# Kernel tuning notes

Measured on AMD Instinct MI355X. Metric: run time of the kernel, lower is better.

The kernel has to match this reference:

```python
import jax, jax.numpy as jnp
import numpy as np

NHEAD = 4
DIM = 256

def rotate_half(x):
    # interleaved: out[..., ::2] = -x[..., 1::2]; out[..., 1::2] = x[..., ::2]
    xe = x[..., ::2]
    xo = x[..., 1::2]
    return jnp.stack([-xo, xe], axis=-1).reshape(x.shape)

def rope_2d(q, k, H, W):
    Dh = q.shape[-1]
    half = Dh // 2
    inv_freq = 1.0 / (10000.0 ** (jnp.arange(half, dtype=jnp.float32) / half))  # [half]
    yy, xx = jnp.meshgrid(jnp.arange(H, dtype=jnp.float32), jnp.arange(W, dtype=jnp.float32), indexing='ij')
    ang_y = yy.reshape(-1)[:, None] * inv_freq  # [N, half]
    ang_x = xx.reshape(-1)[:, None] * inv_freq  # [N, half]
    cy, sy = jnp.cos(ang_y), jnp.sin(ang_y)
    cx, sx = jnp.cos(ang_x), jnp.sin(ang_x)
    def rot(t):
        t1 = t[..., :half]          # y-rotated half
        t2 = t[..., half:2 * half]  # x-rotated half
        ty = t1 * cy + rotate_half(t1) * sy
        tx = t2 * cx + rotate_half(t2) * sx
        return jnp.concatenate([ty, tx, t[..., 2 * half:]], axis=-1)
    return rot(q), rot(k)

def layernorm(x, g, b, eps=1e-5):
    mu = jnp.mean(x, axis=-1, keepdims=True)
    var = jnp.var(x, axis=-1, keepdims=True)
    return (x - mu) / jnp.sqrt(var + eps) * g + b

def setup_inputs() -> dict:
    key = jax.random.key(0)
    ks = jax.random.split(key, 8)
    B, Hs, Ws, C = 4, 48, 48, DIM
    N = Hs * Ws
    s = 0.02
    return {
        'x': jax.random.normal(ks[0], (B, N, C), dtype=jnp.float32),
        'Wqkv': jax.random.normal(ks[1], (3 * C, C), dtype=jnp.float32) * s,
        'Wproj': jax.random.normal(ks[2], (C, C), dtype=jnp.float32) * s,
        'g1': jnp.ones((C,), jnp.float32), 'b1': jnp.zeros((C,), jnp.float32),
        'g2': jnp.ones((C,), jnp.float32), 'b2': jnp.zeros((C,), jnp.float32),
        'W1': jax.random.normal(ks[3], (4 * C, C), dtype=jnp.float32) * s,
        'bf1': jnp.zeros((4 * C,), jnp.float32),
        'W2': jax.random.normal(ks[4], (C, 4 * C), dtype=jnp.float32) * s,
        'bf2': jnp.zeros((C,), jnp.float32),
        'H': Hs, 'W': Ws,
    }

def reference(x, Wqkv, Wproj, g1, b1, g2, b2, W1, bf1, W2, bf2, H, W):
    B, N, C = x.shape
    dh = C // NHEAD
    qkv = (x @ Wqkv.T).reshape(B, N, 3, NHEAD, dh).transpose(2, 0, 3, 1, 4)  # [3,B,h,N,dh]
    q, k, v = qkv[0], qkv[1], qkv[2]
    q, k = rope_2d(q, k, H, W)
    scores = jnp.einsum('bhnd,bhmd->bhnm', q, k) / jnp.sqrt(jnp.float32(dh))
    attn = jax.nn.softmax(scores, axis=-1)  # drop_attn is identity (p=0)
    out = jnp.einsum('bhnm,bhmd->bhnd', attn, v).transpose(0, 2, 1, 3).reshape(B, N, C)
    x = x + out @ Wproj.T
    x = layernorm(x, g1, b1)
    h = jax.nn.gelu(x @ W1.T + bf1, approximate=False)
    x = x + h @ W2.T + bf2
    return layernorm(x, g2, b2)
```

## Files before the change

kernel.cpp:

```cpp
#include <hip/hip_runtime.h>
#include <hip/hip_bf16.h>
#include <math.h>

typedef __hip_bfloat16 bf16;
typedef __attribute__((ext_vector_type(8))) short short8;
typedef __attribute__((ext_vector_type(4))) short short4v;
typedef __attribute__((ext_vector_type(4))) float f32x4;

#define NSEQ 2304
#define CDIM 256
#define NHD  4
#define DH   64

static __device__ __forceinline__ f32x4 mfma_bf16(short8 a, short8 b, f32x4 c) {
  return __builtin_amdgcn_mfma_f32_16x16x32_bf16(a, b, c, 0, 0, 0);
}
static __device__ __forceinline__ short8 ld8(const bf16* p) {
  return *reinterpret_cast<const short8*>(p);
}
static __device__ __forceinline__ short8 lds8(const bf16* p) {
  return *reinterpret_cast<const short8*>(p);
}
static __device__ __forceinline__ float b2f(short v) {
  unsigned int u = ((unsigned int)(unsigned short)v) << 16;
  return __uint_as_float(u);
}
static __device__ __forceinline__ short f2b(float f) {
  bf16 h = __float2bfloat16(f);
  return *reinterpret_cast<short*>(&h);
}

__global__ __launch_bounds__(256) void detect_kernel(const void* __restrict__ xraw,
                                                     int* __restrict__ flag) {
  int t = threadIdx.x;
  const unsigned short* s = (const unsigned short*)xraw;
  int bad = 0;
#pragma unroll
  for (int i = 0; i < 8; ++i) {
    unsigned idx = (((unsigned)(t * 8 + i)) * 9173u) & ((1u << 20) - 1);
    unsigned short v = s[idx * 2];
    unsigned e = (v >> 7) & 0xFFu;
    if (e > 133u) bad++;
  }
  __shared__ int tot;
  if (t == 0) tot = 0;
  __syncthreads();
  atomicAdd(&tot, bad);
  __syncthreads();
  if (t == 0) flag[0] = (tot >= 16) ? 1 : 0;
}

__global__ __launch_bounds__(256) void cvt_all_kernel(const void* sx, const void* sqkv, const void* sproj,
                                                      const void* sw1, const void* sw2,
                                                      const void* g1, const void* b1, const void* g2,
                                                      const void* b2, const void* bias1, const void* bias2,
                                                      bf16* dx, bf16* dqkv, bf16* dproj,
                                                      bf16* dw1, bf16* dw2, bf16* dsm,
                                                      const int* __restrict__ flag) {
  int is32 = flag[0];
  int bid = blockIdx.x;
  const void* src; bf16* dst; int i4;
  if (bid < 2304)      { src = sx;    dst = dx;    i4 = bid * 256 + threadIdx.x; }
  else if (bid < 2496) { src = sqkv;  dst = dqkv;  i4 = (bid - 2304) * 256 + threadIdx.x; }
  else if (bid < 2560) { src = sproj; dst = dproj; i4 = (bid - 2496) * 256 + threadIdx.x; }
  else if (bid < 2816) { src = sw1;   dst = dw1;   i4 = (bid - 2560) * 256 + threadIdx.x; }
  else if (bid < 3072) { src = sw2;   dst = dw2;   i4 = (bid - 2816) * 256 + threadIdx.x; }
  else {
    const void* srcs[6] = {g1, b1, g2, b2, bias1, bias2};
    const int ns[6] = {256, 256, 256, 256, 1024, 256};
    const int off[6] = {0, 256, 512, 768, 1024, 2048};
    int t = threadIdx.x;
#pragma unroll
    for (int j = 0; j < 6; ++j)
      for (int i = t; i < ns[j]; i += 256) {
        if (is32) dsm[off[j] + i] = __float2bfloat16(((const float*)srcs[j])[i]);
        else      dsm[off[j] + i] = ((const bf16*)srcs[j])[i];
      }
    return;
  }
  if (is32) {
    float4 v = ((const float4*)src)[i4];
    short4v o;
    o[0] = f2b(v.x); o[1] = f2b(v.y); o[2] = f2b(v.z); o[3] = f2b(v.w);
    ((short4v*)dst)[i4] = o;
  } else {
    ((short4v*)dst)[i4] = ((const short4v*)src)[i4];
  }
}

__global__ __launch_bounds__(256, 1) void qkv_kernel(const bf16* __restrict__ X,
                                                     const bf16* __restrict__ Wqkv,
                                                     bf16* __restrict__ Q, bf16* __restrict__ K,
                                                     bf16* __restrict__ Vt) {
  int wave = threadIdx.x >> 6, lane = threadIdx.x & 63;
  int l15 = lane & 15, quad = lane >> 4;
  int m0 = (blockIdx.x * 4 + wave) * 64;
  int n0 = blockIdx.y * 64;
  const bf16* arow = X + (size_t)(m0 + l15) * CDIM + quad * 8;
  const bf16* brow = Wqkv + (size_t)(n0 + l15) * CDIM + quad * 8;
  f32x4 z = {0.f, 0.f, 0.f, 0.f};
  f32x4 acc[4][4];
#pragma unroll
  for (int j = 0; j < 4; ++j)
#pragma unroll
    for (int i = 0; i < 4; ++i) acc[j][i] = z;

  short8 a[4], b[4];
#pragma unroll
  for (int i = 0; i < 4; ++i) a[i] = ld8(arow + (size_t)i * 16 * CDIM);
#pragma unroll
  for (int j = 0; j < 4; ++j) b[j] = ld8(brow + (size_t)j * 16 * CDIM);
#pragma unroll
  for (int kk = 32; kk <= CDIM; kk += 32) {
    short8 an[4], bn[4];
    if (kk < CDIM) {
#pragma unroll
      for (int i = 0; i < 4; ++i) an[i] = ld8(arow + (size_t)i * 16 * CDIM + kk);
#pragma unroll
      for (int j = 0; j < 4; ++j) bn[j] = ld8(brow + (size_t)j * 16 * CDIM + kk);
    }
#pragma unroll
    for (int j = 0; j < 4; ++j)
#pragma unroll
      for (int i = 0; i < 4; ++i) acc[j][i] = mfma_bf16(b[j], a[i], acc[j][i]);
    if (kk < CDIM) {
#pragma unroll
      for (int i = 0; i < 4; ++i) a[i] = an[i];
#pragma unroll
      for (int j = 0; j < 4; ++j) b[j] = bn[j];
    }
  }

  int which = n0 >> 8, h = (n0 & 255) >> 6;
#pragma unroll
  for (int j = 0; j < 4; ++j) {
    int d0 = j * 16 + quad * 4;
#pragma unroll
    for (int i = 0; i < 4; ++i) {
      int gm = m0 + i * 16 + l15;
      int bb = gm / NSEQ, n = gm % NSEQ;
      int bh = bb * NHD + h;
      short4v ov;
#pragma unroll
      for (int r = 0; r < 4; ++r) ov[r] = f2b(acc[j][i][r]);
      if (which == 0)
        *reinterpret_cast<short4v*>(Q + ((size_t)bh * NSEQ + n) * DH + d0) = ov;
      else if (which == 1)
        *reinterpret_cast<short4v*>(K + ((size_t)bh * NSEQ + n) * DH + d0) = ov;
      else {
#pragma unroll
        for (int r = 0; r < 4; ++r)
          Vt[((size_t)bh * DH + d0 + r) * NSEQ + n] = __float2bfloat16(acc[j][i][r]);
      }
    }
  }
}

__global__ __launch_bounds__(256) void rope_kernel(bf16* __restrict__ Q, bf16* __restrict__ K,
                                                   const int* __restrict__ Wp) {
  int Wv = Wp[0];
  if (Wv <= 0 || Wv > 65536) Wv = 48;
  int t = blockIdx.x * 256 + threadIdx.x;
  int p = t & 31;
  int row = t >> 5;
  int which = (row >= 16 * NSEQ) ? 1 : 0;
  int r2 = which ? row - 16 * NSEQ : row;
  int bh = r2 / NSEQ, n = r2 % NSEQ;
  int py = n / Wv, px = n - py * Wv;
  int part = p >> 4, i = p & 15;
  float pos = (float)(part ? px : py);
  int j0 = 2 * i;
  const float c = -9.210340371976184f / 32.0f;
  float f0 = expf(c * (float)j0);
  float f1 = expf(c * (float)(j0 + 1));
  float s0, c0, s1, c1;
  sincosf(pos * f0, &s0, &c0);
  sincosf(pos * f1, &s1, &c1);
  bf16* base = (which ? K : Q) + ((size_t)bh * NSEQ + n) * DH + part * 32 + j0;
  float a  = __bfloat162float(base[0]);
  float bb = __bfloat162float(base[1]);
  base[0] = __float2bfloat16(a * c0 - bb * s0);
  base[1] = __float2bfloat16(bb * c1 + a * s1);
}

__global__ __launch_bounds__(256) void attn_kernel(const bf16* __restrict__ Q, const bf16* __restrict__ K,
                                                   const bf16* __restrict__ Vt, bf16* __restrict__ AO) {
  int bh = blockIdx.x, qt = blockIdx.y;
  int tid = threadIdx.x;
  int wave = tid >> 6, lane = tid & 63;
  int l15 = lane & 15, quad = lane >> 4;
  int m0 = qt * 64 + wave * 16;
  const bf16* Qb = Q + (size_t)bh * NSEQ * DH;
  const bf16* Kb = K + (size_t)bh * NSEQ * DH;
  const bf16* Vb = Vt + (size_t)bh * DH * NSEQ;

  __shared__ __align__(16) bf16 kbuf[2][64 * 72];
  __shared__ __align__(16) bf16 vbuf[2][64 * 72];
  __shared__ __align__(16) bf16 plds[4][16 * 72];

  int i1 = tid, i2 = tid + 256;
  int r1 = i1 >> 3, s1 = (i1 & 7) * 8;
  int r2 = i2 >> 3, s2 = (i2 & 7) * 8;

  short8 bq0 = ld8(Qb + (size_t)(m0 + l15) * DH + quad * 8);
  short8 bq1 = ld8(Qb + (size_t)(m0 + l15) * DH + 32 + quad * 8);
#pragma unroll
  for (int i = 0; i < 8; ++i) {
    bq0[i] = f2b(b2f(bq0[i]) * 0.125f);
    bq1[i] = f2b(b2f(bq1[i]) * 0.125f);
  }

  f32x4 z = {0.f, 0.f, 0.f, 0.f};
  f32x4 o[4] = {z, z, z, z};
  float m_run = -1e30f, l_run = 0.f;
  bf16* pb = plds[wave];

  {
    short8 ka = ld8(Kb + (size_t)r1 * DH + s1);
    short8 kb2 = ld8(Kb + (size_t)r2 * DH + s2);
    short8 va = ld8(Vb + (size_t)r1 * NSEQ + s1);
    short8 vb2 = ld8(Vb + (size_t)r2 * NSEQ + s2);
    *reinterpret_cast<short8*>(kbuf[0] + r1 * 72 + s1) = ka;
    *reinterpret_cast<short8*>(kbuf[0] + r2 * 72 + s2) = kb2;
    *reinterpret_cast<short8*>(vbuf[0] + r1 * 72 + s1) = va;
    *reinterpret_cast<short8*>(vbuf[0] + r2 * 72 + s2) = vb2;
  }
  __syncthreads();

  for (int it = 0; it < NSEQ / 64; ++it) {
    int cur = it & 1;
    bool more = (it + 1 < NSEQ / 64);
    short8 ka, kb2, va, vb2;
    if (more) {
      int kc = (it + 1) * 64;
      ka  = ld8(Kb + (size_t)(kc + r1) * DH + s1);
      kb2 = ld8(Kb + (size_t)(kc + r2) * DH + s2);
      va  = ld8(Vb + (size_t)r1 * NSEQ + kc + s1);
      vb2 = ld8(Vb + (size_t)r2 * NSEQ + kc + s2);
    }

    const bf16* kb = kbuf[cur];
    const bf16* vb = vbuf[cur];

    f32x4 s[4];
#pragma unroll
    for (int kt = 0; kt < 4; ++kt) {
      const bf16* kp = kb + (size_t)(kt * 16 + l15) * 72 + quad * 8;
      s[kt] = mfma_bf16(lds8(kp), bq0, z);
      s[kt] = mfma_bf16(lds8(kp + 32), bq1, s[kt]);
    }
    float mx = s[0][0];
#pragma unroll
    for (int kt = 0; kt < 4; ++kt)
#pragma unroll
      for (int r = 0; r < 4; ++r) mx = fmaxf(mx, s[kt][r]);
    mx = fmaxf(mx, __shfl_xor(mx, 16));
    mx = fmaxf(mx, __shfl_xor(mx, 32));
    float m_new = fmaxf(m_run, mx);
    float alpha = __expf(m_run - m_new);
    m_run = m_new;

    float ls = 0.f;
#pragma unroll
    for (int kt = 0; kt < 4; ++kt) {
      float p0 = __expf(s[kt][0] - m_new);
      float p1 = __expf(s[kt][1] - m_new);
      float p2 = __expf(s[kt][2] - m_new);
      float p3 = __expf(s[kt][3] - m_new);
      ls += (p0 + p1) + (p2 + p3);
      short4v pk;
      pk[0] = f2b(p0); pk[1] = f2b(p1); pk[2] = f2b(p2); pk[3] = f2b(p3);
      *reinterpret_cast<short4v*>(pb + l15 * 72 + kt * 16 + quad * 4) = pk;
    }
    l_run = l_run * alpha + ls;
#pragma unroll
    for (int t = 0; t < 4; ++t)
#pragma unroll
      for (int r = 0; r < 4; ++r) o[t][r] *= alpha;

#pragma unroll
    for (int kt2 = 0; kt2 < 2; ++kt2) {
      short8 pfrag = lds8(pb + l15 * 72 + kt2 * 32 + quad * 8);
#pragma unroll
      for (int t = 0; t < 4; ++t) {
        short8 av = lds8(vb + (size_t)(t * 16 + l15) * 72 + kt2 * 32 + quad * 8);
        o[t] = mfma_bf16(av, pfrag, o[t]);
      }
    }

    if (more) {
      bf16* kn = kbuf[1 - cur];
      bf16* vn = vbuf[1 - cur];
      *reinterpret_cast<short8*>(kn + r1 * 72 + s1) = ka;
      *reinterpret_cast<short8*>(kn + r2 * 72 + s2) = kb2;
      *reinterpret_cast<short8*>(vn + r1 * 72 + s1) = va;
      *reinterpret_cast<short8*>(vn + r2 * 72 + s2) = vb2;
    }
    __syncthreads();
  }

  l_run += __shfl_xor(l_run, 16);
  l_run += __shfl_xor(l_run, 32);
  float inv = 1.f / l_run;
  int b = bh >> 2, h = bh & 3;
  bf16* orow = AO + ((size_t)b * NSEQ + (m0 + l15)) * CDIM + h * DH;
#pragma unroll
  for (int t = 0; t < 4; ++t) {
    short4v ov;
#pragma unroll
    for (int r = 0; r < 4; ++r) ov[r] = f2b(o[t][r] * inv);
    *reinterpret_cast<short4v*>(orow + t * 16 + quad * 4) = ov;
  }
}

template <int KD, int EPI>
__global__ __launch_bounds__(256) void gemmS(const bf16* __restrict__ A, const bf16* __restrict__ Wm,
                                             const bf16* __restrict__ bias, const bf16* __restrict__ res,
                                             bf16* __restrict__ outp, int NC) {
  constexpr int KS = KD / 32;
  int tid = threadIdx.x;
  int wave = tid >> 6, lane = tid & 63;
  int l15 = lane & 15, quad = lane >> 4;
  int m0 = (blockIdx.x * 4 + wave) * 16;
  int n0 = blockIdx.y * 64;

  __shared__ __align__(16) bf16 wbuf[2][64 * 40];

  int wr = tid >> 2, wsub = (tid & 3) * 8;
  const bf16* wg = Wm + (size_t)(n0 + wr) * KD + wsub;
  const bf16* arow = A + (size_t)(m0 + l15) * KD + quad * 8;

  f32x4 z = {0.f, 0.f, 0.f, 0.f};
  f32x4 acc[4] = {z, z, z, z};

  *reinterpret_cast<short8*>(wbuf[0] + wr * 40 + wsub) = ld8(wg);
  short8 a_cur = ld8(arow);
  __syncthreads();

  for (int s = 0; s < KS; ++s) {
    int cur = s & 1;
    bool more = (s + 1 < KS);
    short8 wnx, anx;
    if (more) {
      wnx = ld8(wg + (s + 1) * 32);
      anx = ld8(arow + (s + 1) * 32);
    }
    short8 bf[4];
#pragma unroll
    for (int j = 0; j < 4; ++j)
      bf[j] = lds8(wbuf[cur] + (size_t)(j * 16 + l15) * 40 + quad * 8);
#pragma unroll
    for (int j = 0; j < 4; ++j)
      acc[j] = mfma_bf16(bf[j], a_cur, acc[j]);
    if (more) {
      *reinterpret_cast<short8*>(wbuf[1 - cur] + wr * 40 + wsub) = wnx;
      a_cur = anx;
    }
    __syncthreads();
  }

#pragma unroll
  for (int j = 0; j < 4; ++j) {
    int col0 = n0 + j * 16 + quad * 4;
    float bb4[4];
    if (EPI != 0) {
      short4v bl = *reinterpret_cast<const short4v*>(bias + col0);
#pragma unroll
      for (int r = 0; r < 4; ++r) bb4[r] = b2f(bl[r]);
    }
    size_t idx = (size_t)(m0 + l15) * NC + col0;
    short4v ov;
    if (EPI == 0) {
      short4v rl = *reinterpret_cast<const short4v*>(res + idx);
#pragma unroll
      for (int r = 0; r < 4; ++r) ov[r] = f2b(acc[j][r] + b2f(rl[r]));
    } else if (EPI == 1) {
#pragma unroll
      for (int r = 0; r < 4; ++r) {
        float hv = acc[j][r] + bb4[r];
        ov[r] = f2b(0.5f * hv * (1.f + erff(hv * 0.70710678118f)));
      }
    } else {
      short4v rl = *reinterpret_cast<const short4v*>(res + idx);
#pragma unroll
      for (int r = 0; r < 4; ++r) ov[r] = f2b(acc[j][r] + bb4[r] + b2f(rl[r]));
    }
    *reinterpret_cast<short4v*>(outp + idx) = ov;
  }
}

__global__ __launch_bounds__(256) void ln_kernel(const bf16* __restrict__ X, const bf16* __restrict__ g,
                                                 const bf16* __restrict__ bv, bf16* __restrict__ out) {
  int row = blockIdx.x * 4 + (threadIdx.x >> 6);
  int lane = threadIdx.x & 63;
  short4v raw = *reinterpret_cast<const short4v*>(X + (size_t)row * CDIM + lane * 4);
  float vv[4];
  float s = 0.f, sq = 0.f;
#pragma unroll
  for (int i = 0; i < 4; ++i) {
    float f = b2f(raw[i]);
    vv[i] = f; s += f; sq += f * f;
  }
#pragma unroll
  for (int off = 1; off < 64; off <<= 1) { s += __shfl_xor(s, off); sq += __shfl_xor(sq, off); }
  float mu = s * (1.f / CDIM);
  float var = sq * (1.f / CDIM) - mu * mu;
  float rstd = rsqrtf(var + 1e-5f);
#pragma unroll
  for (int i = 0; i < 4; ++i) {
    int c = lane * 4 + i;
    out[(size_t)row * CDIM + c] =
        __float2bfloat16((vv[i] - mu) * rstd * __bfloat162float(g[c]) + __bfloat162float(bv[c]));
  }
}

__global__ __launch_bounds__(256) void ln_out_kernel(const bf16* __restrict__ X, const bf16* __restrict__ g,
                                                     const bf16* __restrict__ bv, void* __restrict__ out,
                                                     const int* __restrict__ flag) {
  int is32 = flag[0];
  int row = blockIdx.x * 4 + (threadIdx.x >> 6);
  int lane = threadIdx.x & 63;
  short4v raw = *reinterpret_cast<const short4v*>(X + (size_t)row * CDIM + lane * 4);
  float vv[4];
  float s = 0.f, sq = 0.f;
#pragma unroll
  for (int i = 0; i < 4; ++i) {
    float f = b2f(raw[i]);
    vv[i] = f; s += f; sq += f * f;
  }
#pragma unroll
  for (int off = 1; off < 64; off <<= 1) { s += __shfl_xor(s, off); sq += __shfl_xor(sq, off); }
  float mu = s * (1.f / CDIM);
  float var = sq * (1.f / CDIM) - mu * mu;
  float rstd = rsqrtf(var + 1e-5f);
#pragma unroll
  for (int i = 0; i < 4; ++i) {
    int c = lane * 4 + i;
    size_t idx = (size_t)row * CDIM + c;
    float v = (vv[i] - mu) * rstd * __bfloat162float(g[c]) + __bfloat162float(bv[c]);
    if (is32) ((float*)out)[idx] = v;
    else      ((bf16*)out)[idx] = __float2bfloat16(v);
  }
}

extern "C" void kernel_launch(void* const* d_in, const int* in_sizes, int n_in,
                              void* d_out, int out_size, void* d_ws, size_t ws_size,
                              hipStream_t stream) {
  const int* Wp = (const int*)d_in[12];

  char* ws = (char*)d_ws;
  const size_t SZ = 4718592;
  bf16* Qc  = (bf16*)(ws + 0 * SZ);
  bf16* Kc  = (bf16*)(ws + 1 * SZ);
  bf16* Vt  = (bf16*)(ws + 2 * SZ);
  bf16* AO  = (bf16*)(ws + 3 * SZ);
  bf16* F   = (bf16*)(ws + 4 * SZ);
  bf16* Y   = (bf16*)(ws + 5 * SZ);
  bf16* xc  = (bf16*)(ws + 6 * SZ);
  bf16* G   = (bf16*)(ws + 0);
  bf16* Wqkvc  = (bf16*)(ws + 7 * SZ);
  bf16* Wprojc = (bf16*)(ws + 7 * SZ + 393216);
  bf16* W1c    = (bf16*)(ws + 7 * SZ + 524288);
  bf16* W2c    = (bf16*)(ws + 7 * SZ + 1048576);
  bf16* smallc = (bf16*)(ws + 7 * SZ + 1572864);
  bf16* g1c  = smallc + 0;
  bf16* b1c  = smallc + 256;
  bf16* g2c  = smallc + 512;
  bf16* b2c  = smallc + 768;
  bf16* bf1c = smallc + 1024;
  bf16* bf2c = smallc + 2048;
  int*  flagp = (int*)(ws + 7 * SZ + 1581568);
  bf16* outsc = (bf16*)d_out;

  detect_kernel<<<1, 256, 0, stream>>>(d_in[0], flagp);
  cvt_all_kernel<<<3073, 256, 0, stream>>>(d_in[0], d_in[1], d_in[2], d_in[7], d_in[9],
                                           d_in[3], d_in[4], d_in[5], d_in[6], d_in[8], d_in[10],
                                           xc, Wqkvc, Wprojc, W1c, W2c, smallc, flagp);

  qkv_kernel<<<dim3(36, 12), 256, 0, stream>>>(xc, Wqkvc, Qc, Kc, Vt);
  rope_kernel<<<9216, 256, 0, stream>>>(Qc, Kc, Wp);
  attn_kernel<<<dim3(16, 36), 256, 0, stream>>>(Qc, Kc, Vt, AO);
  gemmS<256, 0><<<dim3(144, 4), 256, 0, stream>>>(AO, Wprojc, nullptr, xc, outsc, 256);
  ln_kernel<<<2304, 256, 0, stream>>>(outsc, g1c, b1c, F);
  gemmS<256, 1><<<dim3(144, 16), 256, 0, stream>>>(F, W1c, bf1c, nullptr, G, 1024);
  gemmS<1024, 2><<<dim3(144, 4), 256, 0, stream>>>(G, W2c, bf2c, F, Y, 256);
  ln_out_kernel<<<2304, 256, 0, stream>>>(Y, g2c, b2c, d_out, flagp);
}
```

Before: 239.6 us.

## Double query rows per attention wave and add full-K GEMM for K=256

The attention kernel now has each wave process 32 query rows (two 16-row tiles) instead of 16. Each K/V tile loaded into shared memory is reused across twice as many queries, and the grid is halved. A new gemmF kernel stages the whole 64x256 weight slab in LDS once and keeps all A fragments in registers, which removes the double-buffered k-loop for the K=256 projection and FC1 GEMMs. The price is more registers and LDS per block, and fewer attention blocks (288), which may lower occupancy on a chip with many CUs.

```diff
diff --git a/kernel.cpp b/kernel.cpp
--- a/kernel.cpp
+++ b/kernel.cpp
@@ -189,31 +189,38 @@
   int tid = threadIdx.x;
   int wave = tid >> 6, lane = tid & 63;
   int l15 = lane & 15, quad = lane >> 4;
-  int m0 = qt * 64 + wave * 16;
+  int m0 = qt * 128 + wave * 32;
   const bf16* Qb = Q + (size_t)bh * NSEQ * DH;
   const bf16* Kb = K + (size_t)bh * NSEQ * DH;
   const bf16* Vb = Vt + (size_t)bh * DH * NSEQ;
 
   __shared__ __align__(16) bf16 kbuf[2][64 * 72];
   __shared__ __align__(16) bf16 vbuf[2][64 * 72];
-  __shared__ __align__(16) bf16 plds[4][16 * 72];
+  __shared__ __align__(16) bf16 plds[4][2][16 * 72];
 
   int i1 = tid, i2 = tid + 256;
   int r1 = i1 >> 3, s1 = (i1 & 7) * 8;
   int r2 = i2 >> 3, s2 = (i2 & 7) * 8;
 
-  short8 bq0 = ld8(Qb + (size_t)(m0 + l15) * DH + quad * 8);
-  short8 bq1 = ld8(Qb + (size_t)(m0 + l15) * DH + 32 + quad * 8);
-#pragma unroll
-  for (int i = 0; i < 8; ++i) {
-    bq0[i] = f2b(b2f(bq0[i]) * 0.125f);
-    bq1[i] = f2b(b2f(bq1[i]) * 0.125f);
+  short8 bq[2][2];
+#pragma unroll
+  for (int t2 = 0; t2 < 2; ++t2) {
+    bq[t2][0] = ld8(Qb + (size_t)(m0 + t2 * 16 + l15) * DH + quad * 8);
+    bq[t2][1] = ld8(Qb + (size_t)(m0 + t2 * 16 + l15) * DH + 32 + quad * 8);
+#pragma unroll
+    for (int i = 0; i < 8; ++i) {
+      bq[t2][0][i] = f2b(b2f(bq[t2][0][i]) * 0.125f);
+      bq[t2][1][i] = f2b(b2f(bq[t2][1][i]) * 0.125f);
+    }
   }
 
   f32x4 z = {0.f, 0.f, 0.f, 0.f};
-  f32x4 o[4] = {z, z, z, z};
-  float m_run = -1e30f, l_run = 0.f;
-  bf16* pb = plds[wave];
+  f32x4 o[2][4];
+  float m_run[2] = {-1e30f, -1e30f}, l_run[2] = {0.f, 0.f};
+#pragma unroll
+  for (int t2 = 0; t2 < 2; ++t2)
+#pragma unroll
+    for (int t = 0; t < 4; ++t) o[t2][t] = z;
 
   {
     short8 ka = ld8(Kb + (size_t)r1 * DH + s1);
@@ -242,49 +249,60 @@
     const bf16* kb = kbuf[cur];
     const bf16* vb = vbuf[cur];
 
-    f32x4 s[4];
+    f32x4 s[2][4];
 #pragma unroll
     for (int kt = 0; kt < 4; ++kt) {
       const bf16* kp = kb + (size_t)(kt * 16 + l15) * 72 + quad * 8;
-      s[kt] = mfma_bf16(lds8(kp), bq0, z);
-      s[kt] = mfma_bf16(lds8(kp + 32), bq1, s[kt]);
-    }
-    float mx = s[0][0];
-#pragma unroll
-    for (int kt = 0; kt < 4; ++kt)
-#pragma unroll
-      for (int r = 0; r < 4; ++r) mx = fmaxf(mx, s[kt][r]);
-    mx = fmaxf(mx, __shfl_xor(mx, 16));
-    mx = fmaxf(mx, __shfl_xor(mx, 32));
-    float m_new = fmaxf(m_run, mx);
-    float alpha = __expf(m_run - m_new);
-    m_run = m_new;
-
-    float ls = 0.f;
-#pragma unroll
-    for (int kt = 0; kt < 4; ++kt) {
-      float p0 = __expf(s[kt][0] - m_new);
-      float p1 = __expf(s[kt][1] - m_new);
-      float p2 = __expf(s[kt][2] - m_new);
-      float p3 = __expf(s[kt][3] - m_new);
-      ls += (p0 + p1) + (p2 + p3);
-      short4v pk;
-      pk[0] = f2b(p0); pk[1] = f2b(p1); pk[2] = f2b(p2); pk[3] = f2b(p3);
-      *reinterpret_cast<short4v*>(pb + l15 * 72 + kt * 16 + quad * 4) = pk;
-    }
-    l_run = l_run * alpha + ls;
-#pragma unroll
-    for (int t = 0; t < 4; ++t)
-#pragma unroll
-      for (int r = 0; r < 4; ++r) o[t][r] *= alpha;
+      short8 k0 = lds8(kp);
+      short8 k1 = lds8(kp + 32);
+      s[0][kt] = mfma_bf16(k0, bq[0][0], z);
+      s[0][kt] = mfma_bf16(k1, bq[0][1], s[0][kt]);
+      s[1][kt] = mfma_bf16(k0, bq[1][0], z);
+      s[1][kt] = mfma_bf16(k1, bq[1][1], s[1][kt]);
+    }
+
+#pragma unroll
+    for (int t2 = 0; t2 < 2; ++t2) {
+      float mx = s[t2][0][0];
+#pragma unroll
+      for (int kt = 0; kt < 4; ++kt)
+#pragma unroll
+        for (int r = 0; r < 4; ++r) mx = fmaxf(mx, s[t2][kt][r]);
+      mx = fmaxf(mx, __shfl_xor(mx, 16));
+      mx = fmaxf(mx, __shfl_xor(mx, 32));
+      float m_new = fmaxf(m_run[t2], mx);
+      float alpha = __expf(m_run[t2] - m_new);
+      m_run[t2] = m_new;
+
+      float ls = 0.f;
+      bf16* pb = plds[wave][t2];
+#pragma unroll
+      for (int kt = 0; kt < 4; ++kt) {
+        float p0 = __expf(s[t2][kt][0] - m_new);
+        float p1 = __expf(s[t2][kt][1] - m_new);
+        float p2 = __expf(s[t2][kt][2] - m_new);
+        float p3 = __expf(s[t2][kt][3] - m_new);
+        ls += (p0 + p1) + (p2 + p3);
+        short4v pk;
+        pk[0] = f2b(p0); pk[1] = f2b(p1); pk[2] = f2b(p2); pk[3] = f2b(p3);
+        *reinterpret_cast<short4v*>(pb + l15 * 72 + kt * 16 + quad * 4) = pk;
+      }
+      l_run[t2] = l_run[t2] * alpha + ls;
+#pragma unroll
+      for (int t = 0; t < 4; ++t)
+#pragma unroll
+        for (int r = 0; r < 4; ++r) o[t2][t][r] *= alpha;
+    }
 
 #pragma unroll
     for (int kt2 = 0; kt2 < 2; ++kt2) {
-      short8 pfrag = lds8(pb + l15 * 72 + kt2 * 32 + quad * 8);
+      short8 pfA = lds8(plds[wave][0] + l15 * 72 + kt2 * 32 + quad * 8);
+      short8 pfB = lds8(plds[wave][1] + l15 * 72 + kt2 * 32 + quad * 8);
 #pragma unroll
       for (int t = 0; t < 4; ++t) {
         short8 av = lds8(vb + (size_t)(t * 16 + l15) * 72 + kt2 * 32 + quad * 8);
-        o[t] = mfma_bf16(av, pfrag, o[t]);
+        o[0][t] = mfma_bf16(av, pfA, o[0][t]);
+        o[1][t] = mfma_bf16(av, pfB, o[1][t]);
       }
     }
 
@@ -299,17 +317,86 @@
     __syncthreads();
   }
 
-  l_run += __shfl_xor(l_run, 16);
-  l_run += __shfl_xor(l_run, 32);
-  float inv = 1.f / l_run;
   int b = bh >> 2, h = bh & 3;
-  bf16* orow = AO + ((size_t)b * NSEQ + (m0 + l15)) * CDIM + h * DH;
-#pragma unroll
-  for (int t = 0; t < 4; ++t) {
+#pragma unroll
+  for (int t2 = 0; t2 < 2; ++t2) {
+    float l = l_run[t2];
+    l += __shfl_xor(l, 16);
+    l += __shfl_xor(l, 32);
+    float inv = 1.f / l;
+    bf16* orow = AO + ((size_t)b * NSEQ + (m0 + t2 * 16 + l15)) * CDIM + h * DH;
+#pragma unroll
+    for (int t = 0; t < 4; ++t) {
+      short4v ov;
+#pragma unroll
+      for (int r = 0; r < 4; ++r) ov[r] = f2b(o[t2][t][r] * inv);
+      *reinterpret_cast<short4v*>(orow + t * 16 + quad * 4) = ov;
+    }
+  }
+}
+
+template <int EPI>
+__global__ __launch_bounds__(256) void gemmF(const bf16* __restrict__ A, const bf16* __restrict__ Wm,
+                                             const bf16* __restrict__ bias, const bf16* __restrict__ res,
+                                             bf16* __restrict__ outp, int NC) {
+  int tid = threadIdx.x;
+  int wave = tid >> 6, lane = tid & 63;
+  int l15 = lane & 15, quad = lane >> 4;
+  int m0 = (blockIdx.x * 4 + wave) * 16;
+  int n0 = blockIdx.y * 64;
+
+  __shared__ __align__(16) bf16 wbuf[64 * 264];
+
+#pragma unroll
+  for (int r = 0; r < 8; ++r) {
+    int p = tid + 256 * r;
+    int row = p >> 5, col = (p & 31) * 8;
+    *reinterpret_cast<short8*>(wbuf + row * 264 + col) = ld8(Wm + (size_t)(n0 + row) * 256 + col);
+  }
+  const bf16* arow = A + (size_t)(m0 + l15) * 256 + quad * 8;
+  short8 a[8];
+#pragma unroll
+  for (int s = 0; s < 8; ++s) a[s] = ld8(arow + s * 32);
+  __syncthreads();
+
+  f32x4 z = {0.f, 0.f, 0.f, 0.f};
+  f32x4 acc[4] = {z, z, z, z};
+#pragma unroll
+  for (int s = 0; s < 8; ++s) {
+#pragma unroll
+    for (int j = 0; j < 4; ++j) {
+      short8 w = lds8(wbuf + (size_t)(j * 16 + l15) * 264 + s * 32 + quad * 8);
+      acc[j] = mfma_bf16(w, a[s], acc[j]);
+    }
+  }
+
+#pragma unroll
+  for (int j = 0; j < 4; ++j) {
+    int col0 = n0 + j * 16 + quad * 4;
+    float bb4[4];
+    if (EPI != 0) {
+      short4v bl = *reinterpret_cast<const short4v*>(bias + col0);
+#pragma unroll
+      for (int r = 0; r < 4; ++r) bb4[r] = b2f(bl[r]);
+    }
+    size_t idx = (size_t)(m0 + l15) * NC + col0;
     short4v ov;
-#pragma unroll
-    for (int r = 0; r < 4; ++r) ov[r] = f2b(o[t][r] * inv);
-    *reinterpret_cast<short4v*>(orow + t * 16 + quad * 4) = ov;
+    if (EPI == 0) {
+      short4v rl = *reinterpret_cast<const short4v*>(res + idx);
+#pragma unroll
+      for (int r = 0; r < 4; ++r) ov[r] = f2b(acc[j][r] + b2f(rl[r]));
+    } else if (EPI == 1) {
+#pragma unroll
+      for (int r = 0; r < 4; ++r) {
+        float hv = acc[j][r] + bb4[r];
+        ov[r] = f2b(0.5f * hv * (1.f + erff(hv * 0.70710678118f)));
+      }
+    } else {
+      short4v rl = *reinterpret_cast<const short4v*>(res + idx);
+#pragma unroll
+      for (int r = 0; r < 4; ++r) ov[r] = f2b(acc[j][r] + bb4[r] + b2f(rl[r]));
+    }
+    *reinterpret_cast<short4v*>(outp + idx) = ov;
   }
 }
 
@@ -479,10 +566,10 @@
 
   qkv_kernel<<<dim3(36, 12), 256, 0, stream>>>(xc, Wqkvc, Qc, Kc, Vt);
   rope_kernel<<<9216, 256, 0, stream>>>(Qc, Kc, Wp);
-  attn_kernel<<<dim3(16, 36), 256, 0, stream>>>(Qc, Kc, Vt, AO);
-  gemmS<256, 0><<<dim3(144, 4), 256, 0, stream>>>(AO, Wprojc, nullptr, xc, outsc, 256);
+  attn_kernel<<<dim3(16, 18), 256, 0, stream>>>(Qc, Kc, Vt, AO);
+  gemmF<0><<<dim3(144, 4), 256, 0, stream>>>(AO, Wprojc, nullptr, xc, outsc, 256);
   ln_kernel<<<2304, 256, 0, stream>>>(outsc, g1c, b1c, F);
-  gemmS<256, 1><<<dim3(144, 16), 256, 0, stream>>>(F, W1c, bf1c, nullptr, G, 1024);
+  gemmF<1><<<dim3(144, 16), 256, 0, stream>>>(F, W1c, bf1c, nullptr, G, 1024);
   gemmS<1024, 2><<<dim3(144, 4), 256, 0, stream>>>(G, W2c, bf2c, F, Y, 256);
   ln_out_kernel<<<2304, 256, 0, stream>>>(Y, g2c, b2c, d_out, flagp);
 }
```

Result: slower. 251.5 us (+5.0%).

## Replace 64x64 GEMM tiles with 2D-warp 128-wide tiles sharing LDS A and B

Applied to the files above, without the earlier changes.

Replaces the per-wave 16-row GEMM, which stages only the weight tile in LDS, with a block tile of up to 128x128. Both A and B tiles are staged in double-buffered LDS, and waves are laid out in a 2x2 grid, each computing TI x 4 MFMA sub-tiles. The aim is more data reuse per global load and more MFMAs per LDS fetch in the projection and both MLP GEMMs. In exchange it uses more registers and LDS per block and launches fewer blocks, which may lower occupancy and parallelism on the smaller GEMMs.

```diff
diff --git a/kernel.cpp b/kernel.cpp
--- a/kernel.cpp
+++ b/kernel.cpp
@@ -313,79 +313,107 @@
   }
 }
 
-template <int KD, int EPI>
-__global__ __launch_bounds__(256) void gemmS(const bf16* __restrict__ A, const bf16* __restrict__ Wm,
-                                             const bf16* __restrict__ bias, const bf16* __restrict__ res,
-                                             bf16* __restrict__ outp, int NC) {
+template <int KD, int EPI, int TI>
+__global__ __launch_bounds__(256) void gemm128(const bf16* __restrict__ A, const bf16* __restrict__ Wm,
+                                               const bf16* __restrict__ bias, const bf16* __restrict__ res,
+                                               bf16* __restrict__ outp, int NC) {
   constexpr int KS = KD / 32;
+  constexpr int AR = TI * 32;
   int tid = threadIdx.x;
   int wave = tid >> 6, lane = tid & 63;
   int l15 = lane & 15, quad = lane >> 4;
-  int m0 = (blockIdx.x * 4 + wave) * 16;
-  int n0 = blockIdx.y * 64;
-
-  __shared__ __align__(16) bf16 wbuf[2][64 * 40];
-
-  int wr = tid >> 2, wsub = (tid & 3) * 8;
-  const bf16* wg = Wm + (size_t)(n0 + wr) * KD + wsub;
-  const bf16* arow = A + (size_t)(m0 + l15) * KD + quad * 8;
+  int wm = (wave >> 1) * (TI * 16);
+  int wn = (wave & 1) * 64;
+  int m0 = blockIdx.x * AR;
+  int n0 = blockIdx.y * 128;
+
+  __shared__ __align__(16) bf16 abuf[2][AR * 40];
+  __shared__ __align__(16) bf16 bbuf[2][128 * 40];
+
+  int sr = tid >> 2, sc = (tid & 3) * 8;
+
+  const bf16* ag[TI / 2];
+#pragma unroll
+  for (int u = 0; u < TI / 2; ++u) ag[u] = A + (size_t)(m0 + sr + u * 64) * KD + sc;
+  const bf16* bg0 = Wm + (size_t)(n0 + sr) * KD + sc;
+  const bf16* bg1 = Wm + (size_t)(n0 + 64 + sr) * KD + sc;
 
   f32x4 z = {0.f, 0.f, 0.f, 0.f};
-  f32x4 acc[4] = {z, z, z, z};
-
-  *reinterpret_cast<short8*>(wbuf[0] + wr * 40 + wsub) = ld8(wg);
-  short8 a_cur = ld8(arow);
+  f32x4 acc[4][TI];
+#pragma unroll
+  for (int j = 0; j < 4; ++j)
+#pragma unroll
+    for (int i = 0; i < TI; ++i) acc[j][i] = z;
+
+#pragma unroll
+  for (int u = 0; u < TI / 2; ++u)
+    *reinterpret_cast<short8*>(abuf[0] + (sr + u * 64) * 40 + sc) = ld8(ag[u]);
+  *reinterpret_cast<short8*>(bbuf[0] + sr * 40 + sc) = ld8(bg0);
+  *reinterpret_cast<short8*>(bbuf[0] + (64 + sr) * 40 + sc) = ld8(bg1);
   __syncthreads();
 
   for (int s = 0; s < KS; ++s) {
     int cur = s & 1;
     bool more = (s + 1 < KS);
-    short8 wnx, anx;
+    short8 anx[TI / 2], bnx0, bnx1;
     if (more) {
-      wnx = ld8(wg + (s + 1) * 32);
-      anx = ld8(arow + (s + 1) * 32);
-    }
-    short8 bf[4];
+#pragma unroll
+      for (int u = 0; u < TI / 2; ++u) anx[u] = ld8(ag[u] + (s + 1) * 32);
+      bnx0 = ld8(bg0 + (s + 1) * 32);
+      bnx1 = ld8(bg1 + (s + 1) * 32);
+    }
+    short8 af[TI], bf_[4];
+#pragma unroll
+    for (int i = 0; i < TI; ++i)
+      af[i] = lds8(abuf[cur] + (size_t)(wm + i * 16 + l15) * 40 + quad * 8);
 #pragma unroll
     for (int j = 0; j < 4; ++j)
-      bf[j] = lds8(wbuf[cur] + (size_t)(j * 16 + l15) * 40 + quad * 8);
+      bf_[j] = lds8(bbuf[cur] + (size_t)(wn + j * 16 + l15) * 40 + quad * 8);
 #pragma unroll
     for (int j = 0; j < 4; ++j)
-      acc[j] = mfma_bf16(bf[j], a_cur, acc[j]);
+#pragma unroll
+      for (int i = 0; i < TI; ++i)
+        acc[j][i] = mfma_bf16(bf_[j], af[i], acc[j][i]);
     if (more) {
-      *reinterpret_cast<short8*>(wbuf[1 - cur] + wr * 40 + wsub) = wnx;
-      a_cur = anx;
+#pragma unroll
+      for (int u = 0; u < TI / 2; ++u)
+        *reinterpret_cast<short8*>(abuf[1 - cur] + (sr + u * 64) * 40 + sc) = anx[u];
+      *reinterpret_cast<short8*>(bbuf[1 - cur] + sr * 40 + sc) = bnx0;
+      *reinterpret_cast<short8*>(bbuf[1 - cur] + (64 + sr) * 40 + sc) = bnx1;
     }
     __syncthreads();
   }
 
 #pragma unroll
   for (int j = 0; j < 4; ++j) {
-    int col0 = n0 + j * 16 + quad * 4;
+    int col0 = n0 + wn + j * 16 + quad * 4;
     float bb4[4];
     if (EPI != 0) {
       short4v bl = *reinterpret_cast<const short4v*>(bias + col0);
 #pragma unroll
       for (int r = 0; r < 4; ++r) bb4[r] = b2f(bl[r]);
     }
-    size_t idx = (size_t)(m0 + l15) * NC + col0;
-    short4v ov;
-    if (EPI == 0) {
-      short4v rl = *reinterpret_cast<const short4v*>(res + idx);
-#pragma unroll
-      for (int r = 0; r < 4; ++r) ov[r] = f2b(acc[j][r] + b2f(rl[r]));
-    } else if (EPI == 1) {
-#pragma unroll
-      for (int r = 0; r < 4; ++r) {
-        float hv = acc[j][r] + bb4[r];
-        ov[r] = f2b(0.5f * hv * (1.f + erff(hv * 0.70710678118f)));
+#pragma unroll
+    for (int i = 0; i < TI; ++i) {
+      size_t idx = (size_t)(m0 + wm + i * 16 + l15) * NC + col0;
+      short4v ov;
+      if (EPI == 0) {
+        short4v rl = *reinterpret_cast<const short4v*>(res + idx);
+#pragma unroll
+        for (int r = 0; r < 4; ++r) ov[r] = f2b(acc[j][i][r] + b2f(rl[r]));
+      } else if (EPI == 1) {
+#pragma unroll
+        for (int r = 0; r < 4; ++r) {
+          float hv = acc[j][i][r] + bb4[r];
+          ov[r] = f2b(0.5f * hv * (1.f + erff(hv * 0.70710678118f)));
+        }
+      } else {
+        short4v rl = *reinterpret_cast<const short4v*>(res + idx);
+#pragma unroll
+        for (int r = 0; r < 4; ++r) ov[r] = f2b(acc[j][i][r] + bb4[r] + b2f(rl[r]));
       }
-    } else {
-      short4v rl = *reinterpret_cast<const short4v*>(res + idx);
-#pragma unroll
-      for (int r = 0; r < 4; ++r) ov[r] = f2b(acc[j][r] + bb4[r] + b2f(rl[r]));
-    }
-    *reinterpret_cast<short4v*>(outp + idx) = ov;
+      *reinterpret_cast<short4v*>(outp + idx) = ov;
+    }
   }
 }
 
@@ -480,9 +508,9 @@
   qkv_kernel<<<dim3(36, 12), 256, 0, stream>>>(xc, Wqkvc, Qc, Kc, Vt);
   rope_kernel<<<9216, 256, 0, stream>>>(Qc, Kc, Wp);
   attn_kernel<<<dim3(16, 36), 256, 0, stream>>>(Qc, Kc, Vt, AO);
-  gemmS<256, 0><<<dim3(144, 4), 256, 0, stream>>>(AO, Wprojc, nullptr, xc, outsc, 256);
+  gemm128<256, 0, 2><<<dim3(144, 2), 256, 0, stream>>>(AO, Wprojc, nullptr, xc, outsc, 256);
   ln_kernel<<<2304, 256, 0, stream>>>(outsc, g1c, b1c, F);
-  gemmS<256, 1><<<dim3(144, 16), 256, 0, stream>>>(F, W1c, bf1c, nullptr, G, 1024);
-  gemmS<1024, 2><<<dim3(144, 4), 256, 0, stream>>>(G, W2c, bf2c, F, Y, 256);
+  gemm128<256, 1, 4><<<dim3(72, 8), 256, 0, stream>>>(F, W1c, bf1c, nullptr, G, 1024);
+  gemm128<1024, 2, 2><<<dim3(144, 2), 256, 0, stream>>>(G, W2c, bf2c, F, Y, 256);
   ln_out_kernel<<<2304, 256, 0, stream>>>(Y, g2c, b2c, d_out, flagp);
 }
```

Result: no change. 241.6 us (+0.8%).
